# Optimization experiments

Hardware: AMD Instinct MI355X
Metric: run time of the kernel (lower is better)

The kernel has to match this reference:

```python
import jax, jax.numpy as jnp
import numpy as np

NUM_BRANCH = 4
KERNEL_SIZES = (1, 3, 5, 7)
NUM_CLASSES = 1000
IN_C = 256
OUT_C = 256


def _cond_conv(x, w, emb, y):
    # x: [B,C,H,W], w: [O,I,k,k], emb: [num_classes,O], y: [B]
    out = jax.lax.conv_general_dilated(
        x, w, window_strides=(1, 1), padding='SAME',
        dimension_numbers=('NCHW', 'OIHW', 'NCHW'))
    return out + emb[y][:, :, None, None]


def setup_inputs() -> dict:
    key = jax.random.key(0)
    ks = jax.random.split(key, 2 + 2 * NUM_BRANCH)
    B, H = 64, 32
    inp = {
        'x': jax.random.normal(ks[0], (B, IN_C, H, H), dtype=jnp.float32),
        'y': jax.random.randint(ks[1], (B,), 0, NUM_CLASSES, dtype=jnp.int64),
        'sample_arc': jax.random.randint(jax.random.fold_in(key, 7), (B,), 0, NUM_BRANCH, dtype=jnp.int64),
    }
    for i, k in enumerate(KERNEL_SIZES):
        fan_in = IN_C * k * k
        inp[f'w{i}'] = jax.random.normal(ks[2 + 2 * i], (OUT_C, IN_C, k, k), dtype=jnp.float32) / np.sqrt(fan_in)
        inp[f'e{i}'] = jax.random.normal(ks[3 + 2 * i], (NUM_CLASSES, OUT_C), dtype=jnp.float32) * 0.02
    return inp


def reference(x, y, sample_arc, w0, w1, w2, w3, e0, e1, e2, e3):
    ws = (w0, w1, w2, w3)
    es = (e0, e1, e2, e3)
    # Compute every branch for every sample (as the original module does),
    # stack along branch dim: [B, num_branch, O, H, W]
    branch_out = jnp.stack([_cond_conv(x, w, e, y) for w, e in zip(ws, es)], axis=1)
    onehot = jax.nn.one_hot(sample_arc, NUM_BRANCH, dtype=x.dtype)  # [B, num_branch]
    # mask-and-sum (one-hot multiply then reduce over branch dim)
    return jnp.einsum('bn,bnchw->bchw', onehot, branch_out)
```

## Files before the change

### kernel.cpp

```cpp
#include <hip/hip_runtime.h>


typedef unsigned short ushort_t;
typedef __attribute__((ext_vector_type(8))) short short8;
typedef __attribute__((ext_vector_type(4))) float f32x4;

#define CIN   256
#define COUT  256
#define HH    32
#define WW    32
#define HW    1024

#define XT_ELEMS   16777216
#define WT_OFF_0   0
#define WT_OFF_1   65536
#define WT_OFF_2   655360
#define WT_OFF_3   2293760
#define WT_ELEMS   5505024
#define TILE_BYTE_OFF ((size_t)(XT_ELEMS + WT_ELEMS) * 2)
#define MAX_TILES  1024
#define WS_NEEDED  (TILE_BYTE_OFF + MAX_TILES * 2 + 64)

#define XS_R_STRIDE 1520
#define XS_C_STRIDE 40
#define XS_ROWS_MAX 10
#define XS_ELEMS    15200

__device__ inline ushort_t f2bf(float f) {
    unsigned x = __builtin_bit_cast(unsigned, f);
    unsigned r = (x + 0x7FFFu + ((x >> 16) & 1u)) >> 16;
    return (ushort_t)r;
}

__global__ __launch_bounds__(256) void prep_kernel(
    const float* __restrict__ x,
    const float* __restrict__ w0, const float* __restrict__ w1,
    const float* __restrict__ w2, const float* __restrict__ w3,
    const int* __restrict__ arc,
    ushort_t* __restrict__ xt, ushort_t* __restrict__ wt,
    ushort_t* __restrict__ tiles, unsigned* __restrict__ cnt) {
    __shared__ float lds[2 * 32 * 49];
    const int blk = blockIdx.x;
    const int tid = threadIdx.x;

    if (blk < 4096) {
        const int a   = blk >> 10;
        const int cc  = (blk >> 7) & 7;
        const int oc0 = (blk & 127) * 2;
        const int kk  = (a == 0) ? 1 : (a == 1) ? 9 : (a == 2) ? 25 : 49;
        const float* __restrict__ w = (a == 0) ? w0 : (a == 1) ? w1
                                    : (a == 2) ? w2 : w3;
        const size_t woff = (a == 0) ? WT_OFF_0 : (a == 1) ? WT_OFF_1
                          : (a == 2) ? WT_OFF_2 : WT_OFF_3;
        const int ckk = 32 * kk;
#pragma unroll
        for (int ocq = 0; ocq < 2; ++ocq) {
            const float* src = w + ((size_t)((oc0 + ocq) * CIN + cc * 32)) * kk;
            for (int i = tid; i < ckk; i += 256) lds[ocq * ckk + i] = src[i];
        }
        __syncthreads();
        ushort_t* dst = wt + woff + ((size_t)(cc * COUT + oc0)) * kk * 32;
        const int F = 2 * kk * 32;
        for (int j = tid; j < F; j += 256) {
            const int ci  = j & 31;
            const int t2  = j >> 5;
            const int khw = t2 % kk;
            const int ocq = t2 / kk;
            dst[j] = f2bf(lds[ocq * ckk + ci * kk + khw]);
        }
    } else if (blk < 6144) {
        const int id = (blk - 4096) * 256 + tid;
        const int hw = id & 1023;
        const int cc = (id >> 10) & 7;
        const int b  = id >> 13;
        const float* src = x + ((size_t)(b * CIN + cc * 32)) * HW + hw;
        ushort_t* dst = xt + ((size_t)((b * 8 + cc) * HW + hw)) * 32;
#pragma unroll
        for (int v = 0; v < 4; ++v) {
            short8 o;
#pragma unroll
            for (int j = 0; j < 8; ++j)
                o[j] = (short)f2bf(src[(size_t)(v * 8 + j) * HW]);
            *(short8*)(dst + v * 8) = o;
        }
    } else if (tid < 64) {
        const int lane = tid;
        const int ab = (int)arc[lane];
        unsigned long long m[4];
#pragma unroll
        for (int v = 0; v < 4; ++v) m[v] = __ballot(ab == v);
        int gt = 0;
#pragma unroll
        for (int v = 1; v < 4; ++v) if (v > ab) gt += __popcll(m[v]);
        const unsigned long long eq = (ab == 0) ? m[0] : (ab == 1) ? m[1]
                                    : (ab == 2) ? m[2] : m[3];
        const unsigned long long lower = (lane == 0) ? 0ull
                                       : (~0ull >> (64 - lane));
        const int rank = gt + __popcll(eq & lower);
        const int nh   = __popcll(m[2]) + __popcll(m[3]);
        const bool heavy = (ab >= 2);
        const int myCnt = heavy ? 16 : 8;
        const int start = heavy ? 16 * rank : 16 * nh + 8 * (rank - nh);
        for (int j = 0; j < myCnt; ++j)
            tiles[start + j] = (ushort_t)((lane << 5) | j);
        if (lane == 0) { cnt[0] = 0u; cnt[1] = (unsigned)(512 + 8 * nh); }
    }
}

template <int K, int ROWS>
__device__ void conv_body(const ushort_t* __restrict__ xt,
                          const ushort_t* __restrict__ wtb,
                          const float* __restrict__ eb,
                          int b, int cls, int oc0, int r0,
                          float* __restrict__ out, ushort_t* xs) {
    constexpr int KK    = K * K;
    constexpr int PAD   = K / 2;
    constexpr int R     = ROWS + 2 * PAD;
    constexpr int NF    = ROWS;
    constexpr int HROWS = ROWS / 2;
    constexpr int ITER  = (R * 128) / 256;

    const int tid  = threadIdx.x;
    const int wave = tid >> 6;
    const int lane = tid & 63;
    const int wm   = wave >> 1;
    const int wn   = wave & 1;
    const int ln   = lane & 15;
    const int q    = lane >> 4;

    f32x4 acc[4][NF];
#pragma unroll
    for (int mt = 0; mt < 4; ++mt)
#pragma unroll
        for (int nt = 0; nt < NF; ++nt) acc[mt][nt] = (f32x4)0.0f;

    const size_t CCS = (size_t)COUT * KK * 32;
    const ushort_t* wcol = wtb + ((size_t)(oc0 + wm * 64 + ln)) * (KK * 32) + q * 8;
    short8 afp[4];
#pragma unroll
    for (int mt = 0; mt < 4; ++mt)
        afp[mt] = *(const short8*)&wcol[(size_t)(mt * 16 * KK) * 32];

    const ushort_t* xsrc = xt + ((size_t)b * 8) * (HW * 32);

    for (int cc = 0; cc < 8; ++cc) {
        __syncthreads();
#pragma unroll
        for (int i = 0; i < ITER; ++i) {
            const int id = tid + i * 256;
            const int r  = id >> 7;
            const int gw = (id >> 2) & 31;
            const int g4 = id & 3;
            const int gr = r0 - PAD + r;
            short8 v = (short8)0;
            if (gr >= 0 && gr < HH)
                v = *(const short8*)&xsrc[((size_t)(cc * HW + gr * WW + gw)) * 32 + g4 * 8];
            *(short8*)&xs[r * XS_R_STRIDE + (gw + 3) * XS_C_STRIDE + g4 * 8] = v;
        }
        __syncthreads();

        const ushort_t* wb = wcol + (size_t)cc * CCS;
#pragma unroll 1
        for (int kh = 0; kh < K; ++kh) {
#pragma unroll
            for (int kw = 0; kw < K; ++kw) {
                const int khw = kh * K + kw;
                short8 afc[4];
#pragma unroll
                for (int mt = 0; mt < 4; ++mt) afc[mt] = afp[mt];
                {
                    int nkhw = khw + 1;
                    const ushort_t* nb = wb;
                    if (nkhw == KK) { nkhw = 0; if (cc < 7) nb = wb + CCS; }
#pragma unroll
                    for (int mt = 0; mt < 4; ++mt)
                        afp[mt] = *(const short8*)&nb[(size_t)(mt * 16 * KK + nkhw) * 32];
                }
                short8 bf[NF];
#pragma unroll
                for (int nt = 0; nt < NF; ++nt) {
                    const int rl = wn * HROWS + (nt >> 1) + kh;
                    const int c  = (nt & 1) * 16 + ln + 3 + (kw - PAD);
                    bf[nt] = *(const short8*)&xs[rl * XS_R_STRIDE + c * XS_C_STRIDE + q * 8];
                }
#pragma unroll
                for (int mt = 0; mt < 4; ++mt)
#pragma unroll
                    for (int nt = 0; nt < NF; ++nt)
                        acc[mt][nt] = __builtin_amdgcn_mfma_f32_16x16x32_bf16(
                            afc[mt], bf[nt], acc[mt][nt], 0, 0, 0);
            }
        }
    }

#pragma unroll
    for (int mt = 0; mt < 4; ++mt) {
#pragma unroll
        for (int i = 0; i < 4; ++i) {
            const int oc = oc0 + wm * 64 + mt * 16 + q * 4 + i;
            const float ev = eb[(size_t)cls * COUT + oc];
            float* ob = out + ((size_t)(b * COUT + oc)) * HW;
#pragma unroll
            for (int nt = 0; nt < NF; ++nt) {
                const int row = r0 + wn * HROWS + (nt >> 1);
                const int col = (nt & 1) * 16 + ln;
                ob[row * WW + col] = acc[mt][nt][i] + ev;
            }
        }
    }
}

__global__ __launch_bounds__(256, 2) void conv_mfma(
    const ushort_t* __restrict__ xt, const ushort_t* __restrict__ wt,
    const int* __restrict__ y, const int* __restrict__ arc,
    const float* __restrict__ e0, const float* __restrict__ e1,
    const float* __restrict__ e2, const float* __restrict__ e3,
    float* __restrict__ out,
    const ushort_t* __restrict__ tiles, unsigned* __restrict__ cnt) {
    __shared__ ushort_t xs[XS_ELEMS];
    __shared__ int t_sh;
    const int tid = threadIdx.x;
    const unsigned T = cnt[1];

    for (int i = tid; i < 240; i += 256) {
        const int g    = i & 3;
        const int cell = i >> 2;
        const int cidx = cell % 6;
        const int r    = cell / 6;
        const int col  = (cidx < 3) ? cidx : cidx + 32;
        *(short8*)&xs[r * XS_R_STRIDE + col * XS_C_STRIDE + g * 8] = (short8)0;
    }

    for (;;) {
        if (tid == 0) {
            const unsigned t = atomicAdd(cnt, 1u);
            t_sh = (t < T) ? (int)tiles[t] : -1;
        }
        __syncthreads();
        const int e = t_sh;
        __syncthreads();
        if (e < 0) break;

        const int b   = e >> 5;
        const int j   = e & 31;
        const int oc0 = (j & 1) << 7;
        const int a   = __builtin_amdgcn_readfirstlane(arc[b]);
        const int cls = __builtin_amdgcn_readfirstlane(y[b]);
        switch (a) {
            case 0:  conv_body<1, 8>(xt, wt + WT_OFF_0, e0, b, cls, oc0,
                                     (j >> 1) << 3, out, xs); break;
            case 1:  conv_body<3, 8>(xt, wt + WT_OFF_1, e1, b, cls, oc0,
                                     (j >> 1) << 3, out, xs); break;
            case 2:  conv_body<5, 4>(xt, wt + WT_OFF_2, e2, b, cls, oc0,
                                     (j >> 1) << 2, out, xs); break;
            default: conv_body<7, 4>(xt, wt + WT_OFF_3, e3, b, cls, oc0,
                                     (j >> 1) << 2, out, xs); break;
        }
    }
}

__global__ __launch_bounds__(256) void cond_conv_direct(
    const float* __restrict__ x, const int* __restrict__ y,
    const int* __restrict__ arc,
    const float* __restrict__ w0, const float* __restrict__ e0,
    const float* __restrict__ w1, const float* __restrict__ e1,
    const float* __restrict__ w2, const float* __restrict__ e2,
    const float* __restrict__ w3, const float* __restrict__ e3,
    float* __restrict__ out) {
    const int b   = blockIdx.x >> 4;
    const int o0  = (blockIdx.x & 15) << 4;
    const int tid = threadIdx.x;
    const int col  = tid & 31;
    const int row0 = tid >> 5;
    int a   = __builtin_amdgcn_readfirstlane(arc[b]);
    int cls = __builtin_amdgcn_readfirstlane(y[b]);
    const int k   = (a == 0) ? 1 : (a == 1) ? 3 : (a == 2) ? 5 : 7;
    const int kk  = k * k;
    const int pad = k >> 1;
    const float* __restrict__ wp = (a == 0) ? w0 : (a == 1) ? w1 : (a == 2) ? w2 : w3;
    const float* __restrict__ ep = (a == 0) ? e0 : (a == 1) ? e1 : (a == 2) ? e2 : e3;
    __shared__ float xsh[8 * HW];
    float acc[16][4];
#pragma unroll
    for (int o = 0; o < 16; ++o)
#pragma unroll
        for (int p = 0; p < 4; ++p) acc[o][p] = 0.f;
    const float* xb = x + (size_t)b * CIN * HW;
    for (int c0 = 0; c0 < CIN; c0 += 8) {
        __syncthreads();
        const float4* src = (const float4*)(xb + c0 * HW);
        float4* dst = (float4*)xsh;
#pragma unroll
        for (int i = 0; i < 8; ++i) dst[tid + (i << 8)] = src[tid + (i << 8)];
        __syncthreads();
        for (int kh = 0; kh < k; ++kh) {
            const int dh = kh - pad;
            int raddr[4]; bool rok[4];
#pragma unroll
            for (int p = 0; p < 4; ++p) {
                const int rr = row0 + 8 * p + dh;
                rok[p] = (rr >= 0) && (rr < HH);
                raddr[p] = (rok[p] ? rr : 0) * WW;
            }
            for (int kw = 0; kw < k; ++kw) {
                const int cc2 = col + kw - pad;
                const bool cok = (cc2 >= 0) && (cc2 < WW);
                const int cofs = cok ? cc2 : 0;
                const int khw = kh * k + kw;
#pragma unroll
                for (int ci = 0; ci < 8; ++ci) {
                    float xv[4];
#pragma unroll
                    for (int p = 0; p < 4; ++p) {
                        const float v = xsh[ci * HW + raddr[p] + cofs];
                        xv[p] = (rok[p] && cok) ? v : 0.f;
                    }
                    const float* wb = wp + (size_t)o0 * CIN * kk + (size_t)(c0 + ci) * kk + khw;
#pragma unroll
                    for (int o = 0; o < 16; ++o) {
                        const float wsv = wb[(size_t)o * CIN * kk];
#pragma unroll
                        for (int p = 0; p < 4; ++p) acc[o][p] += wsv * xv[p];
                    }
                }
            }
        }
    }
    const float* erow = ep + (size_t)cls * COUT + o0;
    float* ob = out + (size_t)(b * COUT + o0) * HW;
#pragma unroll
    for (int o = 0; o < 16; ++o) {
        const float ev = erow[o];
#pragma unroll
        for (int p = 0; p < 4; ++p)
            ob[o * HW + (row0 + 8 * p) * WW + col] = acc[o][p] + ev;
    }
}

extern "C" void kernel_launch(void* const* d_in, const int* in_sizes, int n_in,
                              void* d_out, int out_size, void* d_ws, size_t ws_size,
                              hipStream_t stream) {
    const float* x   = (const float*)d_in[0];
    const int*   y   = (const int*)  d_in[1];
    const int*   arc = (const int*)  d_in[2];
    const float* w0  = (const float*)d_in[3];
    const float* e0  = (const float*)d_in[4];
    const float* w1  = (const float*)d_in[5];
    const float* e1  = (const float*)d_in[6];
    const float* w2  = (const float*)d_in[7];
    const float* e2  = (const float*)d_in[8];
    const float* w3  = (const float*)d_in[9];
    const float* e3  = (const float*)d_in[10];
    float* out = (float*)d_out;
    const int B = in_sizes[1];

    if (ws_size >= WS_NEEDED && B == 64) {
        ushort_t* xt    = (ushort_t*)d_ws;
        ushort_t* wt    = xt + XT_ELEMS;
        ushort_t* tiles = (ushort_t*)((char*)d_ws + TILE_BYTE_OFF);
        unsigned* cnt   = (unsigned*)((char*)d_ws + TILE_BYTE_OFF + MAX_TILES * 2);
        hipLaunchKernelGGL(prep_kernel, dim3(6145), dim3(256), 0, stream,
                           x, w0, w1, w2, w3, arc, xt, wt, tiles, cnt);
        hipLaunchKernelGGL(conv_mfma, dim3(512), dim3(256), 0, stream,
                           xt, wt, y, arc, e0, e1, e2, e3, out, tiles, cnt);
    } else {
        hipLaunchKernelGGL(cond_conv_direct, dim3(B * 16), dim3(256), 0, stream,
                           x, y, arc, w0, e0, w1, e1, w2, e2, w3, e3, out);
    }
}
```

Before: 398.7 us.

## Shrink conv tiles, use async global-to-LDS loads, raise occupancy

Output tiles shrink to 4 rows with fewer output-channel fragments per wave (MT=4 or 2), which doubles the tile count and grid size and allows 4 blocks per CU. Input staging now uses global_load_lds direct-to-LDS transfers with an unpadded column stride, so LDS use per block drops. The x transpose prep is split across more threads, each writing one 16-byte chunk. The intent is higher occupancy and better load balance across the persistent tile queue. The cost is less weight and input reuse per tile, and possible LDS bank conflicts from removing the column padding.

```diff
diff --git a/kernel.cpp b/kernel.cpp
--- a/kernel.cpp
+++ b/kernel.cpp
@@ -18,18 +18,22 @@
 #define WT_OFF_3   2293760
 #define WT_ELEMS   5505024
 #define TILE_BYTE_OFF ((size_t)(XT_ELEMS + WT_ELEMS) * 2)
-#define MAX_TILES  1024
+#define MAX_TILES  2048
 #define WS_NEEDED  (TILE_BYTE_OFF + MAX_TILES * 2 + 64)
 
-#define XS_R_STRIDE 1520
-#define XS_C_STRIDE 40
-#define XS_ROWS_MAX 10
-#define XS_ELEMS    15200
+#define XS_R_STRIDE 1216
+#define XS_ELEMS    12160
 
 __device__ inline ushort_t f2bf(float f) {
     unsigned x = __builtin_bit_cast(unsigned, f);
     unsigned r = (x + 0x7FFFu + ((x >> 16) & 1u)) >> 16;
     return (ushort_t)r;
+}
+
+__device__ inline void gld16(const ushort_t* g, ushort_t* l) {
+    __builtin_amdgcn_global_load_lds(
+        (const __attribute__((address_space(1))) unsigned int*)g,
+        (__attribute__((address_space(3))) unsigned int*)l, 16, 0, 0);
 }
 
 __global__ __launch_bounds__(256) void prep_kernel(
@@ -68,21 +72,18 @@
             const int ocq = t2 / kk;
             dst[j] = f2bf(lds[ocq * ckk + ci * kk + khw]);
         }
-    } else if (blk < 6144) {
-        const int id = (blk - 4096) * 256 + tid;
-        const int hw = id & 1023;
-        const int cc = (id >> 10) & 7;
-        const int b  = id >> 13;
-        const float* src = x + ((size_t)(b * CIN + cc * 32)) * HW + hw;
-        ushort_t* dst = xt + ((size_t)((b * 8 + cc) * HW + hw)) * 32;
-#pragma unroll
-        for (int v = 0; v < 4; ++v) {
-            short8 o;
-#pragma unroll
-            for (int j = 0; j < 8; ++j)
-                o[j] = (short)f2bf(src[(size_t)(v * 8 + j) * HW]);
-            *(short8*)(dst + v * 8) = o;
-        }
+    } else if (blk < 12288) {
+        const int g  = (blk - 4096) * 256 + tid;
+        const int q8 = g & 3;
+        const int hw = (g >> 2) & 1023;
+        const int cc = (g >> 12) & 7;
+        const int b  = g >> 15;
+        const float* src = x + ((size_t)(b * CIN + cc * 32 + q8 * 8)) * HW + hw;
+        short8 o;
+#pragma unroll
+        for (int j = 0; j < 8; ++j)
+            o[j] = (short)f2bf(src[(size_t)j * HW]);
+        *(short8*)(xt + (size_t)g * 8) = o;
     } else if (tid < 64) {
         const int lane = tid;
         const int ab = (int)arc[lane];
@@ -99,26 +100,23 @@
         const int rank = gt + __popcll(eq & lower);
         const int nh   = __popcll(m[2]) + __popcll(m[3]);
         const bool heavy = (ab >= 2);
-        const int myCnt = heavy ? 16 : 8;
-        const int start = heavy ? 16 * rank : 16 * nh + 8 * (rank - nh);
+        const int myCnt = heavy ? 32 : 16;
+        const int start = heavy ? 32 * rank : 32 * nh + 16 * (rank - nh);
         for (int j = 0; j < myCnt; ++j)
             tiles[start + j] = (ushort_t)((lane << 5) | j);
-        if (lane == 0) { cnt[0] = 0u; cnt[1] = (unsigned)(512 + 8 * nh); }
-    }
-}
-
-template <int K, int ROWS>
+        if (lane == 0) { cnt[0] = 0u; cnt[1] = (unsigned)(1024 + 16 * nh); }
+    }
+}
+
+template <int K, int MT>
 __device__ void conv_body(const ushort_t* __restrict__ xt,
                           const ushort_t* __restrict__ wtb,
                           const float* __restrict__ eb,
                           int b, int cls, int oc0, int r0,
                           float* __restrict__ out, ushort_t* xs) {
-    constexpr int KK    = K * K;
-    constexpr int PAD   = K / 2;
-    constexpr int R     = ROWS + 2 * PAD;
-    constexpr int NF    = ROWS;
-    constexpr int HROWS = ROWS / 2;
-    constexpr int ITER  = (R * 128) / 256;
+    constexpr int KK  = K * K;
+    constexpr int PAD = K / 2;
+    constexpr int R   = 4 + 2 * PAD;
 
     const int tid  = threadIdx.x;
     const int wave = tid >> 6;
@@ -128,17 +126,17 @@
     const int ln   = lane & 15;
     const int q    = lane >> 4;
 
-    f32x4 acc[4][NF];
-#pragma unroll
-    for (int mt = 0; mt < 4; ++mt)
-#pragma unroll
-        for (int nt = 0; nt < NF; ++nt) acc[mt][nt] = (f32x4)0.0f;
-
-    const size_t CCS = (size_t)COUT * KK * 32;
-    const ushort_t* wcol = wtb + ((size_t)(oc0 + wm * 64 + ln)) * (KK * 32) + q * 8;
-    short8 afp[4];
-#pragma unroll
-    for (int mt = 0; mt < 4; ++mt)
+    f32x4 acc[MT][4];
+#pragma unroll
+    for (int mt = 0; mt < MT; ++mt)
+#pragma unroll
+        for (int nt = 0; nt < 4; ++nt) acc[mt][nt] = (f32x4)0.0f;
+
+    const int ocw = oc0 + wm * (MT * 16);
+    const ushort_t* wcol = wtb + ((size_t)(ocw + ln) * KK) * 32 + q * 8;
+    short8 afp[MT];
+#pragma unroll
+    for (int mt = 0; mt < MT; ++mt)
         afp[mt] = *(const short8*)&wcol[(size_t)(mt * 16 * KK) * 32];
 
     const ushort_t* xsrc = xt + ((size_t)b * 8) * (HW * 32);
@@ -146,47 +144,53 @@
     for (int cc = 0; cc < 8; ++cc) {
         __syncthreads();
 #pragma unroll
-        for (int i = 0; i < ITER; ++i) {
-            const int id = tid + i * 256;
-            const int r  = id >> 7;
-            const int gw = (id >> 2) & 31;
-            const int g4 = id & 3;
-            const int gr = r0 - PAD + r;
-            short8 v = (short8)0;
-            if (gr >= 0 && gr < HH)
-                v = *(const short8*)&xsrc[((size_t)(cc * HW + gr * WW + gw)) * 32 + g4 * 8];
-            *(short8*)&xs[r * XS_R_STRIDE + (gw + 3) * XS_C_STRIDE + g4 * 8] = v;
-        }
-        __syncthreads();
-
-        const ushort_t* wb = wcol + (size_t)cc * CCS;
+        for (int i = 0; i < R / 2; ++i) {
+            const int run = i * 4 + wave;
+            const int r   = run >> 1;
+            const int h   = run & 1;
+            const int gr  = r0 - PAD + r;
+            ushort_t* ldst = xs + r * XS_R_STRIDE + 96 + h * 512;
+            if (gr >= 0 && gr < HH) {
+                const ushort_t* src =
+                    xsrc + ((size_t)(cc * HW + gr * WW)) * 32 + h * 512 + lane * 8;
+                gld16(src, ldst);
+            } else {
+                *(short8*)(ldst + lane * 8) = (short8)0;
+            }
+        }
+        __syncthreads();
+
+        const ushort_t* wb = wcol + ((size_t)cc * COUT * KK) * 32;
 #pragma unroll 1
         for (int kh = 0; kh < K; ++kh) {
 #pragma unroll
             for (int kw = 0; kw < K; ++kw) {
                 const int khw = kh * K + kw;
-                short8 afc[4];
-#pragma unroll
-                for (int mt = 0; mt < 4; ++mt) afc[mt] = afp[mt];
+                short8 afc[MT];
+#pragma unroll
+                for (int mt = 0; mt < MT; ++mt) afc[mt] = afp[mt];
                 {
                     int nkhw = khw + 1;
                     const ushort_t* nb = wb;
-                    if (nkhw == KK) { nkhw = 0; if (cc < 7) nb = wb + CCS; }
-#pragma unroll
-                    for (int mt = 0; mt < 4; ++mt)
+                    if (nkhw == KK) {
+                        nkhw = 0;
+                        if (cc < 7) nb = wb + ((size_t)COUT * KK) * 32;
+                    }
+#pragma unroll
+                    for (int mt = 0; mt < MT; ++mt)
                         afp[mt] = *(const short8*)&nb[(size_t)(mt * 16 * KK + nkhw) * 32];
                 }
-                short8 bf[NF];
-#pragma unroll
-                for (int nt = 0; nt < NF; ++nt) {
-                    const int rl = wn * HROWS + (nt >> 1) + kh;
+                short8 bf[4];
+#pragma unroll
+                for (int nt = 0; nt < 4; ++nt) {
+                    const int rl = wn * 2 + (nt >> 1) + kh;
                     const int c  = (nt & 1) * 16 + ln + 3 + (kw - PAD);
-                    bf[nt] = *(const short8*)&xs[rl * XS_R_STRIDE + c * XS_C_STRIDE + q * 8];
+                    bf[nt] = *(const short8*)&xs[rl * XS_R_STRIDE + c * 32 + q * 8];
                 }
 #pragma unroll
-                for (int mt = 0; mt < 4; ++mt)
-#pragma unroll
-                    for (int nt = 0; nt < NF; ++nt)
+                for (int mt = 0; mt < MT; ++mt)
+#pragma unroll
+                    for (int nt = 0; nt < 4; ++nt)
                         acc[mt][nt] = __builtin_amdgcn_mfma_f32_16x16x32_bf16(
                             afc[mt], bf[nt], acc[mt][nt], 0, 0, 0);
             }
@@ -194,15 +198,15 @@
     }
 
 #pragma unroll
-    for (int mt = 0; mt < 4; ++mt) {
+    for (int mt = 0; mt < MT; ++mt) {
 #pragma unroll
         for (int i = 0; i < 4; ++i) {
-            const int oc = oc0 + wm * 64 + mt * 16 + q * 4 + i;
+            const int oc = ocw + mt * 16 + q * 4 + i;
             const float ev = eb[(size_t)cls * COUT + oc];
             float* ob = out + ((size_t)(b * COUT + oc)) * HW;
 #pragma unroll
-            for (int nt = 0; nt < NF; ++nt) {
-                const int row = r0 + wn * HROWS + (nt >> 1);
+            for (int nt = 0; nt < 4; ++nt) {
+                const int row = r0 + wn * 2 + (nt >> 1);
                 const int col = (nt & 1) * 16 + ln;
                 ob[row * WW + col] = acc[mt][nt][i] + ev;
             }
@@ -210,7 +214,7 @@
     }
 }
 
-__global__ __launch_bounds__(256, 2) void conv_mfma(
+__global__ __launch_bounds__(256, 4) void conv_mfma(
     const ushort_t* __restrict__ xt, const ushort_t* __restrict__ wt,
     const int* __restrict__ y, const int* __restrict__ arc,
     const float* __restrict__ e0, const float* __restrict__ e1,
@@ -228,7 +232,7 @@
         const int cidx = cell % 6;
         const int r    = cell / 6;
         const int col  = (cidx < 3) ? cidx : cidx + 32;
-        *(short8*)&xs[r * XS_R_STRIDE + col * XS_C_STRIDE + g * 8] = (short8)0;
+        *(short8*)&xs[r * XS_R_STRIDE + col * 32 + g * 8] = (short8)0;
     }
 
     for (;;) {
@@ -243,18 +247,17 @@
 
         const int b   = e >> 5;
         const int j   = e & 31;
-        const int oc0 = (j & 1) << 7;
         const int a   = __builtin_amdgcn_readfirstlane(arc[b]);
         const int cls = __builtin_amdgcn_readfirstlane(y[b]);
         switch (a) {
-            case 0:  conv_body<1, 8>(xt, wt + WT_OFF_0, e0, b, cls, oc0,
-                                     (j >> 1) << 3, out, xs); break;
-            case 1:  conv_body<3, 8>(xt, wt + WT_OFF_1, e1, b, cls, oc0,
-                                     (j >> 1) << 3, out, xs); break;
-            case 2:  conv_body<5, 4>(xt, wt + WT_OFF_2, e2, b, cls, oc0,
-                                     (j >> 1) << 2, out, xs); break;
-            default: conv_body<7, 4>(xt, wt + WT_OFF_3, e3, b, cls, oc0,
-                                     (j >> 1) << 2, out, xs); break;
+            case 0:  conv_body<1, 4>(xt, wt + WT_OFF_0, e0, b, cls,
+                                     (j & 1) << 7, (j >> 1) << 2, out, xs); break;
+            case 1:  conv_body<3, 4>(xt, wt + WT_OFF_1, e1, b, cls,
+                                     (j & 1) << 7, (j >> 1) << 2, out, xs); break;
+            case 2:  conv_body<5, 2>(xt, wt + WT_OFF_2, e2, b, cls,
+                                     (j & 3) << 6, (j >> 2) << 2, out, xs); break;
+            default: conv_body<7, 2>(xt, wt + WT_OFF_3, e3, b, cls,
+                                     (j & 3) << 6, (j >> 2) << 2, out, xs); break;
         }
     }
 }
@@ -359,9 +362,9 @@
         ushort_t* wt    = xt + XT_ELEMS;
         ushort_t* tiles = (ushort_t*)((char*)d_ws + TILE_BYTE_OFF);
         unsigned* cnt   = (unsigned*)((char*)d_ws + TILE_BYTE_OFF + MAX_TILES * 2);
-        hipLaunchKernelGGL(prep_kernel, dim3(6145), dim3(256), 0, stream,
+        hipLaunchKernelGGL(prep_kernel, dim3(12289), dim3(256), 0, stream,
                            x, w0, w1, w2, w3, arc, xt, wt, tiles, cnt);
-        hipLaunchKernelGGL(conv_mfma, dim3(512), dim3(256), 0, stream,
+        hipLaunchKernelGGL(conv_mfma, dim3(1024), dim3(256), 0, stream,
                            xt, wt, y, arc, e0, e1, e2, e3, out, tiles, cnt);
     } else {
         hipLaunchKernelGGL(cond_conv_direct, dim3(B * 16), dim3(256), 0, stream,
```

Result: slower. 421.8 us (+5.8%).
